# Kernel optimization log

Hardware: AMD Instinct MI355X
Metric: run time of the kernel (lower is better)

## Reference

```python
import jax, jax.numpy as jnp
import numpy as np

VOCAB = 32000
ROUTE_BIAS = 10.0  # weight on the deterministic one-hot route vs mu logits


def setup_inputs() -> dict:
    key = jax.random.key(0)
    k1, k2, k3, k4, k5, k6 = jax.random.split(key, 6)
    B, S, H = 2, 4096, 1024
    E, Ie = 8, 512  # intermediate_size=4096 -> expert_intermediate=512, fused dim=2*Ie=1024
    return {
        "hidden_states": jax.random.normal(k1, (B, S, H), dtype=jnp.float32),
        "token_ids": jax.random.randint(k2, (B, S), 0, VOCAB),
        "mu": jax.random.normal(k3, (B, S, H), dtype=jnp.float32),
        "gate_up_proj": jax.random.normal(k4, (E, H, 2 * Ie), dtype=jnp.float32) * 0.02,
        "down_proj": jax.random.normal(k5, (E, Ie, H), dtype=jnp.float32) * 0.02,
        "mu_router_w": jax.random.normal(k6, (E, H), dtype=jnp.float32) * 0.02,
    }


def reference(hidden_states, token_ids, mu, gate_up_proj, down_proj, mu_router_w):
    B, S, H = hidden_states.shape
    E, _, F2 = gate_up_proj.shape
    Ie = F2 // 2
    N = B * S

    # deterministic token->expert routing, optionally perturbed by mu logits
    token_to_expert = jnp.arange(VOCAB, dtype=jnp.int32) % E
    base_expert = token_to_expert[jnp.clip(token_ids, 0, VOCAB - 1)]      # [B,S]
    mu_logits = jnp.einsum('bsh,eh->bse', mu, mu_router_w)                 # [B,S,E]
    combined = jax.nn.one_hot(base_expert, E, dtype=mu_logits.dtype) * ROUTE_BIAS + mu_logits
    expert_ids = jnp.argmax(combined, axis=-1).reshape(N)                  # [N]

    x = hidden_states.reshape(N, H)
    tok = jnp.arange(N)

    # compute per-expert GEMM then select per-token expert output
    # (same math as gathering the full weight slab per token, without the
    #  N*H*2Ie gathered-weight blowup of the original torch code)
    gu_all = jnp.einsum('nh,ehf->enf', x, gate_up_proj)                    # [E,N,2Ie]
    gu = gu_all[expert_ids, tok]                                           # [N,2Ie]
    gate, up = gu[:, :Ie], gu[:, Ie:]
    inter = jax.nn.silu(gate) * up                                         # [N,Ie]

    z_all = jnp.einsum('ni,eih->enh', inter, down_proj)                    # [E,N,H]
    out = z_all[expert_ids, tok].reshape(B, S, H)
    return out
```

## Files before the change

kernel.cpp:

```cpp
#include <hip/hip_runtime.h>
#include <hip/hip_bf16.h>
#include <stdint.h>

typedef __bf16 bf16x8 __attribute__((ext_vector_type(8)));
typedef float f32x4 __attribute__((ext_vector_type(4)));

#define ROUTE_BIAS_F 10.0f
#define VOCAB_SZ 32000

__device__ __forceinline__ unsigned short f2bf(float f) {
    union { float f; unsigned u; } v; v.f = f;
    unsigned u = v.u;
    unsigned r = u + 0x7FFFu + ((u >> 16) & 1u);
    return (unsigned short)(r >> 16);
}
__device__ __forceinline__ float bf2f(unsigned short s) {
    union { unsigned u; float f; } v; v.u = ((unsigned)s) << 16;
    return v.f;
}
__device__ __forceinline__ void ld16(const unsigned short* g, unsigned short* l) {
    __builtin_amdgcn_global_load_lds(
        (const __attribute__((address_space(1))) void*)g,
        (__attribute__((address_space(3))) void*)l, 16, 0, 0);
}

__global__ void k_convert_bf16(const float* __restrict__ in,
                               unsigned short* __restrict__ out, int n) {
    int i = (blockIdx.x * blockDim.x + threadIdx.x) * 4;
    if (i + 3 < n) {
        float4 f = *(const float4*)(in + i);
        ushort4 o;
        o.x = f2bf(f.x); o.y = f2bf(f.y); o.z = f2bf(f.z); o.w = f2bf(f.w);
        *(ushort4*)(out + i) = o;
    } else {
        for (; i < n; ++i) out[i] = f2bf(in[i]);
    }
}

__global__ void k_transpose_bf16(const float* __restrict__ in,
                                 unsigned short* __restrict__ out, int R, int C) {
    __shared__ float tile[32][33];
    int e = blockIdx.z;
    const float* inp = in + (size_t)e * R * C;
    unsigned short* outp = out + (size_t)e * R * C;
    int c0 = blockIdx.x * 32, r0 = blockIdx.y * 32;
    int tx = threadIdx.x, ty = threadIdx.y;
#pragma unroll
    for (int k = 0; k < 32; k += 8)
        tile[ty + k][tx] = inp[(size_t)(r0 + ty + k) * C + c0 + tx];
    __syncthreads();
#pragma unroll
    for (int k = 0; k < 32; k += 8)
        outp[(size_t)(c0 + ty + k) * R + r0 + tx] = f2bf(tile[tx][ty + k]);
}

__global__ void k_logits(const float* __restrict__ mu, const int* __restrict__ tok_ids,
                         const float* __restrict__ rw, int H, int N,
                         int* __restrict__ eids) {
    int lane = threadIdx.x & 63;
    int wv   = threadIdx.x >> 6;
    int tok  = blockIdx.x * 4 + wv;
    if (tok >= N) return;
    float acc[8];
#pragma unroll
    for (int e = 0; e < 8; ++e) acc[e] = 0.f;
    const float* m = mu + (size_t)tok * H;
    for (int h = lane; h < H; h += 64) {
        float mv = m[h];
#pragma unroll
        for (int e = 0; e < 8; ++e) acc[e] += mv * rw[e * H + h];
    }
#pragma unroll
    for (int e = 0; e < 8; ++e) {
        float v = acc[e];
#pragma unroll
        for (int off = 32; off > 0; off >>= 1) v += __shfl_xor(v, off);
        acc[e] = v;
    }
    if (lane == 0) {
        int t = tok_ids[tok];
        if (t < 0) t = 0;
        if (t > VOCAB_SZ - 1) t = VOCAB_SZ - 1;
        int be = t % 8;
        float best = -1e30f; int bi = 0;
#pragma unroll
        for (int e = 0; e < 8; ++e) {
            float v = acc[e] + (e == be ? ROUTE_BIAS_F : 0.f);
            if (v > best) { best = v; bi = e; }
        }
        eids[tok] = bi;
    }
}

__global__ void k_count(const int* __restrict__ eids,
                        int* __restrict__ blockcnt, int N) {
    __shared__ int cnt[8];
    int tid = threadIdx.x;
    if (tid < 8) cnt[tid] = 0;
    __syncthreads();
    int tok = blockIdx.x * 256 + tid;
    int lane = tid & 63;
    int eid = (tok < N) ? eids[tok] : -1;
#pragma unroll
    for (int e = 0; e < 8; ++e) {
        unsigned long long m = __ballot(eid == e);
        if (lane == 0 && m) atomicAdd(&cnt[e], __popcll(m));
    }
    __syncthreads();
    if (tid < 8) blockcnt[blockIdx.x * 8 + tid] = cnt[tid];
}

__global__ void k_scan(const int* __restrict__ blockcnt,
                       int* __restrict__ counts, int* __restrict__ base_,
                       int* __restrict__ offs, int NB) {
    __shared__ int tot[8];
    int lane = threadIdx.x;
    int e = lane >> 3, g = lane & 7;
    int v[4];
    int s = 0;
#pragma unroll
    for (int i = 0; i < 4; ++i) { v[i] = s; s += blockcnt[(g * 4 + i) * 8 + e]; }
    int inc = s;
#pragma unroll
    for (int d = 1; d < 8; d <<= 1) {
        int t = __shfl_up(inc, d);
        if (g >= d) inc += t;
    }
    int excl = inc - s;
#pragma unroll
    for (int i = 0; i < 4; ++i) offs[(g * 4 + i) * 8 + e] = excl + v[i];
    if (g == 7) { counts[e] = inc; tot[e] = inc; }
    __syncthreads();
    if (lane == 0) {
        int s2 = 0;
#pragma unroll
        for (int i = 0; i < 8; ++i) { base_[i] = s2; s2 += tot[i]; }
    }
}

__global__ void k_scatter(const int* __restrict__ eids,
                          const int* __restrict__ offs,
                          int* __restrict__ list, int N) {
    __shared__ int wavecnt[4][8];
    int tid = threadIdx.x;
    int lane = tid & 63, wv = tid >> 6;
    int tok = blockIdx.x * 256 + tid;
    int eid = (tok < N) ? eids[tok] : -1;
    unsigned long long below = (1ull << lane) - 1ull;
    int myrank = 0;
#pragma unroll
    for (int e = 0; e < 8; ++e) {
        unsigned long long m = __ballot(eid == e);
        if (lane == 0) wavecnt[wv][e] = __popcll(m);
        if (eid == e) myrank = __popcll(m & below);
    }
    __syncthreads();
    if (eid >= 0) {
        int pre = 0;
        for (int w = 0; w < wv; ++w) pre += wavecnt[w][eid];
        int pos = offs[blockIdx.x * 8 + eid] + pre + myrank;
        list[eid * N + pos] = tok;
    }
}

#define TM 64
#define TN 128
#define TK 64

__global__ __launch_bounds__(256, 4) void k_gemm_gateup(
    const unsigned short* __restrict__ X,
    const unsigned short* __restrict__ Wt,
    unsigned short* __restrict__ IT,
    const int* __restrict__ counts, const int* __restrict__ base_,
    const int* __restrict__ list, int N, int H, int Ie) {
    int bid = blockIdx.x;
    int e = bid & 7;
    int t = bid >> 3;
    int nt = t & 7;
    int mt = t >> 3;
    int cnt = counts[e];
    int m0 = mt * TM;
    if (m0 >= cnt) return;
    int F2 = 2 * Ie;

    __shared__ __align__(16) unsigned short As[TM * TK];
    __shared__ __align__(16) unsigned short Bs[TN * TK];

    int tid = threadIdx.x;
    int lane = tid & 63, wv = tid >> 6;
    int wm = (wv >> 1) * 32, wn = (wv & 1) * 64;

    int rowg = lane >> 3;
    int sl   = (lane & 7) ^ rowg;

    const unsigned short* ag[2];
    const unsigned short* bg[4];
#pragma unroll
    for (int i = 0; i < 2; ++i) {
        int r = wv * 16 + i * 8 + rowg;
        int gr = m0 + r;
        int tokrow = (gr < cnt) ? list[e * N + gr] : 0;
        ag[i] = X + (size_t)tokrow * H + sl * 8;
    }
#pragma unroll
    for (int i = 0; i < 4; ++i) {
        int r = wv * 32 + i * 8 + rowg;
        int wrow = (r & 1) * Ie + nt * 64 + (r >> 1);
        bg[i] = Wt + ((size_t)e * F2 + wrow) * H + sl * 8;
    }

    f32x4 acc[2][4];
#pragma unroll
    for (int i = 0; i < 2; ++i)
#pragma unroll
        for (int j = 0; j < 4; ++j) acc[i][j] = (f32x4)(0.f);

    int q = lane >> 4, m = lane & 15;
    int sw = m & 7;

    for (int k0 = 0; k0 < H; k0 += TK) {
#pragma unroll
        for (int i = 0; i < 2; ++i)
            ld16(ag[i] + k0, &As[(wv * 16 + i * 8) * TK]);
#pragma unroll
        for (int i = 0; i < 4; ++i)
            ld16(bg[i] + k0, &Bs[(wv * 32 + i * 8) * TK]);
        __syncthreads();
#pragma unroll
        for (int ks = 0; ks < TK; ks += 32) {
            int kc = ks >> 3;
            int ck = ((kc + q) ^ sw) << 3;
            bf16x8 af[2], bfr[4];
#pragma unroll
            for (int im = 0; im < 2; ++im)
                af[im] = *(const bf16x8*)&As[(wm + m + im * 16) * TK + ck];
#pragma unroll
            for (int in_ = 0; in_ < 4; ++in_)
                bfr[in_] = *(const bf16x8*)&Bs[(wn + m + in_ * 16) * TK + ck];
#pragma unroll
            for (int im = 0; im < 2; ++im)
#pragma unroll
                for (int in_ = 0; in_ < 4; ++in_)
                    acc[im][in_] = __builtin_amdgcn_mfma_f32_16x16x32_bf16(
                        af[im], bfr[in_], acc[im][in_], 0, 0, 0);
        }
        __syncthreads();
    }

    int b = base_[e];
    int nt64 = nt * 64;
#pragma unroll
    for (int im = 0; im < 2; ++im) {
#pragma unroll
        for (int j = 0; j < 4; ++j) {
            int row = wm + im * 16 + q * 4 + j;
            int gr = m0 + row;
#pragma unroll
            for (int in_ = 0; in_ < 4; ++in_) {
                float v = acc[im][in_][j];
                float u = __shfl_xor(v, 1);
                float g = v;
                float s = g / (1.f + __expf(-g));
                float res = s * u;
                if (!(lane & 1) && gr < cnt) {
                    int oc = nt64 + ((wn + in_ * 16 + m) >> 1);
                    IT[(size_t)(b + gr) * Ie + oc] = f2bf(res);
                }
            }
        }
    }
}

__global__ __launch_bounds__(256, 4) void k_gemm_down(
    const unsigned short* __restrict__ IT,
    const unsigned short* __restrict__ Wt,
    float* __restrict__ OUT,
    const int* __restrict__ counts, const int* __restrict__ base_,
    const int* __restrict__ list, int N, int Ie, int H) {
    int bid = blockIdx.x;
    int e = bid & 7;
    int t = bid >> 3;
    int nt = t & 7;
    int mt = t >> 3;
    int cnt = counts[e];
    int m0 = mt * TM;
    if (m0 >= cnt) return;
    int n0 = nt * TN;
    int b = base_[e];

    __shared__ __align__(16) unsigned short As[TM * TK];
    __shared__ __align__(16) unsigned short Bs[TN * TK];

    int tid = threadIdx.x;
    int lane = tid & 63, wv = tid >> 6;
    int wm = (wv >> 1) * 32, wn = (wv & 1) * 64;

    int rowg = lane >> 3;
    int sl   = (lane & 7) ^ rowg;

    const unsigned short* We = Wt + ((size_t)e * H + n0) * Ie;
    const unsigned short* ag[2];
    const unsigned short* bg[4];
#pragma unroll
    for (int i = 0; i < 2; ++i) {
        int r = wv * 16 + i * 8 + rowg;
        int gr = m0 + r;
        int arow = (gr < cnt) ? (b + gr) : b;
        ag[i] = IT + (size_t)arow * Ie + sl * 8;
    }
#pragma unroll
    for (int i = 0; i < 4; ++i) {
        int r = wv * 32 + i * 8 + rowg;
        bg[i] = We + (size_t)r * Ie + sl * 8;
    }

    f32x4 acc[2][4];
#pragma unroll
    for (int i = 0; i < 2; ++i)
#pragma unroll
        for (int j = 0; j < 4; ++j) acc[i][j] = (f32x4)(0.f);

    int q = lane >> 4, m = lane & 15;
    int sw = m & 7;

    for (int k0 = 0; k0 < Ie; k0 += TK) {
#pragma unroll
        for (int i = 0; i < 2; ++i)
            ld16(ag[i] + k0, &As[(wv * 16 + i * 8) * TK]);
#pragma unroll
        for (int i = 0; i < 4; ++i)
            ld16(bg[i] + k0, &Bs[(wv * 32 + i * 8) * TK]);
        __syncthreads();
#pragma unroll
        for (int ks = 0; ks < TK; ks += 32) {
            int kc = ks >> 3;
            int ck = ((kc + q) ^ sw) << 3;
            bf16x8 af[2], bfr[4];
#pragma unroll
            for (int im = 0; im < 2; ++im)
                af[im] = *(const bf16x8*)&As[(wm + m + im * 16) * TK + ck];
#pragma unroll
            for (int in_ = 0; in_ < 4; ++in_)
                bfr[in_] = *(const bf16x8*)&Bs[(wn + m + in_ * 16) * TK + ck];
#pragma unroll
            for (int im = 0; im < 2; ++im)
#pragma unroll
                for (int in_ = 0; in_ < 4; ++in_)
                    acc[im][in_] = __builtin_amdgcn_mfma_f32_16x16x32_bf16(
                        af[im], bfr[in_], acc[im][in_], 0, 0, 0);
        }
        __syncthreads();
    }

#pragma unroll
    for (int im = 0; im < 2; ++im) {
#pragma unroll
        for (int j = 0; j < 4; ++j) {
            int row = wm + im * 16 + q * 4 + j;
            int gr = m0 + row;
            if (gr < cnt) {
                int tok = list[e * N + gr];
                float* orow = OUT + (size_t)tok * H + n0;
#pragma unroll
                for (int in_ = 0; in_ < 4; ++in_) {
                    int col = wn + in_ * 16 + m;
                    orow[col] = acc[im][in_][j];
                }
            }
        }
    }
}

extern "C" void kernel_launch(void* const* d_in, const int* in_sizes, int n_in,
                              void* d_out, int out_size, void* d_ws, size_t ws_size,
                              hipStream_t stream) {
    const float* hidden   = (const float*)d_in[0];
    const int*   tok_ids  = (const int*)d_in[1];
    const float* mu       = (const float*)d_in[2];
    const float* gup      = (const float*)d_in[3];
    const float* dnp      = (const float*)d_in[4];
    const float* rw       = (const float*)d_in[5];
    float* out = (float*)d_out;

    int N  = in_sizes[1];
    int H  = in_sizes[0] / N;
    int E  = in_sizes[5] / H;
    int F2 = in_sizes[3] / (E * H);
    int Ie = F2 / 2;

    int NB = (N + 255) / 256;

    char* ws = (char*)d_ws;
    size_t o = 0;
    auto alloc = [&](size_t sz) {
        size_t r = o;
        o += (sz + 255) & ~(size_t)255;
        return r;
    };
    int* counts   = (int*)(ws + alloc((size_t)E * 4));
    int* base_    = (int*)(ws + alloc((size_t)E * 4));
    int* eids     = (int*)(ws + alloc((size_t)N * 4));
    int* blockcnt = (int*)(ws + alloc((size_t)NB * 8 * 4));
    int* offs     = (int*)(ws + alloc((size_t)NB * 8 * 4));
    int* list     = (int*)(ws + alloc((size_t)E * N * 4));
    unsigned short* xb   = (unsigned short*)(ws + alloc((size_t)N * H * 2));
    unsigned short* wgut = (unsigned short*)(ws + alloc((size_t)E * F2 * H * 2));
    unsigned short* wdnt = (unsigned short*)(ws + alloc((size_t)E * H * Ie * 2));
    unsigned short* it   = (unsigned short*)(ws + alloc((size_t)N * Ie * 2));

    k_convert_bf16<<<dim3((N * H / 4 + 255) / 256), dim3(256), 0, stream>>>(hidden, xb, N * H);

    dim3 tb(32, 8);
    k_transpose_bf16<<<dim3(F2 / 32, H / 32, E), tb, 0, stream>>>(gup, wgut, H, F2);
    k_transpose_bf16<<<dim3(H / 32, Ie / 32, E), tb, 0, stream>>>(dnp, wdnt, Ie, H);

    k_logits<<<dim3((N + 3) / 4), dim3(256), 0, stream>>>(mu, tok_ids, rw, H, N, eids);
    k_count<<<dim3(NB), dim3(256), 0, stream>>>(eids, blockcnt, N);
    k_scan<<<dim3(1), dim3(64), 0, stream>>>(blockcnt, counts, base_, offs, NB);
    k_scatter<<<dim3(NB), dim3(256), 0, stream>>>(eids, offs, list, N);

    int MT = (N + TM - 1) / TM;
    k_gemm_gateup<<<dim3(E * MT * (Ie / 64)), dim3(256), 0, stream>>>(
        xb, wgut, it, counts, base_, list, N, H, Ie);

    k_gemm_down<<<dim3(E * MT * (H / TN)), dim3(256), 0, stream>>>(
        it, wdnt, out, counts, base_, list, N, Ie, H);
}
```

Before: 227.5 us.

## Fuse bf16 convert into router logits, merge transposes, use 2-wave GEMM blocks

Hidden-state bf16 conversion is folded into the router-logit kernel, which now reads mu and the router weights with float4 loads, removing one launch and a separate pass over the activations. The two weight transposes are merged into a single launch covering both weight tensors. Both expert GEMMs move from 4 waves of 32x64 tiles to 2 waves each computing 64x64, doubling per-wave MFMA work and register use and halving threads per block, with launch bounds lowered accordingly. The higher register count may reduce occupancy.

```diff
diff --git a/kernel.cpp b/kernel.cpp
--- a/kernel.cpp
+++ b/kernel.cpp
@@ -24,51 +24,35 @@
         (__attribute__((address_space(3))) void*)l, 16, 0, 0);
 }
 
-__global__ void k_convert_bf16(const float* __restrict__ in,
-                               unsigned short* __restrict__ out, int n) {
-    int i = (blockIdx.x * blockDim.x + threadIdx.x) * 4;
-    if (i + 3 < n) {
-        float4 f = *(const float4*)(in + i);
-        ushort4 o;
-        o.x = f2bf(f.x); o.y = f2bf(f.y); o.z = f2bf(f.z); o.w = f2bf(f.w);
-        *(ushort4*)(out + i) = o;
-    } else {
-        for (; i < n; ++i) out[i] = f2bf(in[i]);
-    }
-}
-
-__global__ void k_transpose_bf16(const float* __restrict__ in,
-                                 unsigned short* __restrict__ out, int R, int C) {
-    __shared__ float tile[32][33];
-    int e = blockIdx.z;
-    const float* inp = in + (size_t)e * R * C;
-    unsigned short* outp = out + (size_t)e * R * C;
-    int c0 = blockIdx.x * 32, r0 = blockIdx.y * 32;
-    int tx = threadIdx.x, ty = threadIdx.y;
-#pragma unroll
-    for (int k = 0; k < 32; k += 8)
-        tile[ty + k][tx] = inp[(size_t)(r0 + ty + k) * C + c0 + tx];
-    __syncthreads();
-#pragma unroll
-    for (int k = 0; k < 32; k += 8)
-        outp[(size_t)(c0 + ty + k) * R + r0 + tx] = f2bf(tile[tx][ty + k]);
-}
-
-__global__ void k_logits(const float* __restrict__ mu, const int* __restrict__ tok_ids,
-                         const float* __restrict__ rw, int H, int N,
-                         int* __restrict__ eids) {
+__global__ void k_prep(const float* __restrict__ hidden, const float* __restrict__ mu,
+                       const int* __restrict__ tok_ids, const float* __restrict__ rw,
+                       unsigned short* __restrict__ xb, int* __restrict__ eids,
+                       int H, int N) {
     int lane = threadIdx.x & 63;
     int wv   = threadIdx.x >> 6;
     int tok  = blockIdx.x * 4 + wv;
     if (tok >= N) return;
+    const float4* hp = (const float4*)(hidden + (size_t)tok * H);
+    const float4* mp = (const float4*)(mu + (size_t)tok * H);
+    const float4* rp = (const float4*)rw;
+    ushort4* xp = (ushort4*)(xb + (size_t)tok * H);
+    int H4 = H >> 2;
     float acc[8];
 #pragma unroll
     for (int e = 0; e < 8; ++e) acc[e] = 0.f;
-    const float* m = mu + (size_t)tok * H;
-    for (int h = lane; h < H; h += 64) {
-        float mv = m[h];
-#pragma unroll
-        for (int e = 0; e < 8; ++e) acc[e] += mv * rw[e * H + h];
+#pragma unroll
+    for (int j = 0; j < 4; ++j) {
+        int idx = lane + 64 * j;
+        float4 h4 = hp[idx];
+        ushort4 o;
+        o.x = f2bf(h4.x); o.y = f2bf(h4.y); o.z = f2bf(h4.z); o.w = f2bf(h4.w);
+        xp[idx] = o;
+        float4 m4 = mp[idx];
+#pragma unroll
+        for (int e = 0; e < 8; ++e) {
+            float4 w4 = rp[e * H4 + idx];
+            acc[e] += m4.x * w4.x + m4.y * w4.y + m4.z * w4.z + m4.w * w4.w;
+        }
     }
 #pragma unroll
     for (int e = 0; e < 8; ++e) {
@@ -90,6 +74,26 @@
         }
         eids[tok] = bi;
     }
+}
+
+__global__ void k_transpose_all(const float* __restrict__ gup, const float* __restrict__ dnp,
+                                unsigned short* __restrict__ wgut, unsigned short* __restrict__ wdnt,
+                                int H, int F2, int Ie) {
+    __shared__ float tile[32][33];
+    int z = blockIdx.z;
+    const float* inp; unsigned short* outp; int R, C;
+    if (z < 8) { R = H; C = F2; inp = gup + (size_t)z * R * C;       outp = wgut + (size_t)z * R * C; }
+    else       { R = Ie; C = H; inp = dnp + (size_t)(z - 8) * R * C; outp = wdnt + (size_t)(z - 8) * R * C; }
+    int c0 = blockIdx.x * 32, r0 = blockIdx.y * 32;
+    if (r0 >= R || c0 >= C) return;
+    int tx = threadIdx.x, ty = threadIdx.y;
+#pragma unroll
+    for (int k = 0; k < 32; k += 8)
+        tile[ty + k][tx] = inp[(size_t)(r0 + ty + k) * C + c0 + tx];
+    __syncthreads();
+#pragma unroll
+    for (int k = 0; k < 32; k += 8)
+        outp[(size_t)(c0 + ty + k) * R + r0 + tx] = f2bf(tile[tx][ty + k]);
 }
 
 __global__ void k_count(const int* __restrict__ eids,
@@ -167,7 +171,7 @@
 #define TN 128
 #define TK 64
 
-__global__ __launch_bounds__(256, 4) void k_gemm_gateup(
+__global__ __launch_bounds__(128, 3) void k_gemm_gateup(
     const unsigned short* __restrict__ X,
     const unsigned short* __restrict__ Wt,
     unsigned short* __restrict__ IT,
@@ -188,30 +192,30 @@
 
     int tid = threadIdx.x;
     int lane = tid & 63, wv = tid >> 6;
-    int wm = (wv >> 1) * 32, wn = (wv & 1) * 64;
+    int wn = wv * 64;
 
     int rowg = lane >> 3;
     int sl   = (lane & 7) ^ rowg;
 
-    const unsigned short* ag[2];
-    const unsigned short* bg[4];
-#pragma unroll
-    for (int i = 0; i < 2; ++i) {
-        int r = wv * 16 + i * 8 + rowg;
+    const unsigned short* ag[4];
+    const unsigned short* bg[8];
+#pragma unroll
+    for (int i = 0; i < 4; ++i) {
+        int r = wv * 32 + i * 8 + rowg;
         int gr = m0 + r;
         int tokrow = (gr < cnt) ? list[e * N + gr] : 0;
         ag[i] = X + (size_t)tokrow * H + sl * 8;
     }
 #pragma unroll
-    for (int i = 0; i < 4; ++i) {
-        int r = wv * 32 + i * 8 + rowg;
+    for (int i = 0; i < 8; ++i) {
+        int r = wv * 64 + i * 8 + rowg;
         int wrow = (r & 1) * Ie + nt * 64 + (r >> 1);
         bg[i] = Wt + ((size_t)e * F2 + wrow) * H + sl * 8;
     }
 
-    f32x4 acc[2][4];
-#pragma unroll
-    for (int i = 0; i < 2; ++i)
+    f32x4 acc[4][4];
+#pragma unroll
+    for (int i = 0; i < 4; ++i)
 #pragma unroll
         for (int j = 0; j < 4; ++j) acc[i][j] = (f32x4)(0.f);
 
@@ -220,25 +224,25 @@
 
     for (int k0 = 0; k0 < H; k0 += TK) {
 #pragma unroll
-        for (int i = 0; i < 2; ++i)
-            ld16(ag[i] + k0, &As[(wv * 16 + i * 8) * TK]);
-#pragma unroll
         for (int i = 0; i < 4; ++i)
-            ld16(bg[i] + k0, &Bs[(wv * 32 + i * 8) * TK]);
+            ld16(ag[i] + k0, &As[(wv * 32 + i * 8) * TK]);
+#pragma unroll
+        for (int i = 0; i < 8; ++i)
+            ld16(bg[i] + k0, &Bs[(wv * 64 + i * 8) * TK]);
         __syncthreads();
 #pragma unroll
         for (int ks = 0; ks < TK; ks += 32) {
             int kc = ks >> 3;
             int ck = ((kc + q) ^ sw) << 3;
-            bf16x8 af[2], bfr[4];
-#pragma unroll
-            for (int im = 0; im < 2; ++im)
-                af[im] = *(const bf16x8*)&As[(wm + m + im * 16) * TK + ck];
+            bf16x8 af[4], bfr[4];
+#pragma unroll
+            for (int im = 0; im < 4; ++im)
+                af[im] = *(const bf16x8*)&As[(m + im * 16) * TK + ck];
 #pragma unroll
             for (int in_ = 0; in_ < 4; ++in_)
                 bfr[in_] = *(const bf16x8*)&Bs[(wn + m + in_ * 16) * TK + ck];
 #pragma unroll
-            for (int im = 0; im < 2; ++im)
+            for (int im = 0; im < 4; ++im)
 #pragma unroll
                 for (int in_ = 0; in_ < 4; ++in_)
                     acc[im][in_] = __builtin_amdgcn_mfma_f32_16x16x32_bf16(
@@ -250,10 +254,10 @@
     int b = base_[e];
     int nt64 = nt * 64;
 #pragma unroll
-    for (int im = 0; im < 2; ++im) {
+    for (int im = 0; im < 4; ++im) {
 #pragma unroll
         for (int j = 0; j < 4; ++j) {
-            int row = wm + im * 16 + q * 4 + j;
+            int row = im * 16 + q * 4 + j;
             int gr = m0 + row;
 #pragma unroll
             for (int in_ = 0; in_ < 4; ++in_) {
@@ -271,7 +275,7 @@
     }
 }
 
-__global__ __launch_bounds__(256, 4) void k_gemm_down(
+__global__ __launch_bounds__(128, 3) void k_gemm_down(
     const unsigned short* __restrict__ IT,
     const unsigned short* __restrict__ Wt,
     float* __restrict__ OUT,
@@ -293,30 +297,30 @@
 
     int tid = threadIdx.x;
     int lane = tid & 63, wv = tid >> 6;
-    int wm = (wv >> 1) * 32, wn = (wv & 1) * 64;
+    int wn = wv * 64;
 
     int rowg = lane >> 3;
     int sl   = (lane & 7) ^ rowg;
 
     const unsigned short* We = Wt + ((size_t)e * H + n0) * Ie;
-    const unsigned short* ag[2];
-    const unsigned short* bg[4];
-#pragma unroll
-    for (int i = 0; i < 2; ++i) {
-        int r = wv * 16 + i * 8 + rowg;
+    const unsigned short* ag[4];
+    const unsigned short* bg[8];
+#pragma unroll
+    for (int i = 0; i < 4; ++i) {
+        int r = wv * 32 + i * 8 + rowg;
         int gr = m0 + r;
         int arow = (gr < cnt) ? (b + gr) : b;
         ag[i] = IT + (size_t)arow * Ie + sl * 8;
     }
 #pragma unroll
-    for (int i = 0; i < 4; ++i) {
-        int r = wv * 32 + i * 8 + rowg;
+    for (int i = 0; i < 8; ++i) {
+        int r = wv * 64 + i * 8 + rowg;
         bg[i] = We + (size_t)r * Ie + sl * 8;
     }
 
-    f32x4 acc[2][4];
-#pragma unroll
-    for (int i = 0; i < 2; ++i)
+    f32x4 acc[4][4];
+#pragma unroll
+    for (int i = 0; i < 4; ++i)
 #pragma unroll
         for (int j = 0; j < 4; ++j) acc[i][j] = (f32x4)(0.f);
 
@@ -325,25 +329,25 @@
 
     for (int k0 = 0; k0 < Ie; k0 += TK) {
 #pragma unroll
-        for (int i = 0; i < 2; ++i)
-            ld16(ag[i] + k0, &As[(wv * 16 + i * 8) * TK]);
-#pragma unroll
         for (int i = 0; i < 4; ++i)
-            ld16(bg[i] + k0, &Bs[(wv * 32 + i * 8) * TK]);
+            ld16(ag[i] + k0, &As[(wv * 32 + i * 8) * TK]);
+#pragma unroll
+        for (int i = 0; i < 8; ++i)
+            ld16(bg[i] + k0, &Bs[(wv * 64 + i * 8) * TK]);
         __syncthreads();
 #pragma unroll
         for (int ks = 0; ks < TK; ks += 32) {
             int kc = ks >> 3;
             int ck = ((kc + q) ^ sw) << 3;
-            bf16x8 af[2], bfr[4];
-#pragma unroll
-            for (int im = 0; im < 2; ++im)
-                af[im] = *(const bf16x8*)&As[(wm + m + im * 16) * TK + ck];
+            bf16x8 af[4], bfr[4];
+#pragma unroll
+            for (int im = 0; im < 4; ++im)
+                af[im] = *(const bf16x8*)&As[(m + im * 16) * TK + ck];
 #pragma unroll
             for (int in_ = 0; in_ < 4; ++in_)
                 bfr[in_] = *(const bf16x8*)&Bs[(wn + m + in_ * 16) * TK + ck];
 #pragma unroll
-            for (int im = 0; im < 2; ++im)
+            for (int im = 0; im < 4; ++im)
 #pragma unroll
                 for (int in_ = 0; in_ < 4; ++in_)
                     acc[im][in_] = __builtin_amdgcn_mfma_f32_16x16x32_bf16(
@@ -353,10 +357,10 @@
     }
 
 #pragma unroll
-    for (int im = 0; im < 2; ++im) {
+    for (int im = 0; im < 4; ++im) {
 #pragma unroll
         for (int j = 0; j < 4; ++j) {
-            int row = wm + im * 16 + q * 4 + j;
+            int row = im * 16 + q * 4 + j;
             int gr = m0 + row;
             if (gr < cnt) {
                 int tok = list[e * N + gr];
@@ -408,21 +412,18 @@
     unsigned short* wdnt = (unsigned short*)(ws + alloc((size_t)E * H * Ie * 2));
     unsigned short* it   = (unsigned short*)(ws + alloc((size_t)N * Ie * 2));
 
-    k_convert_bf16<<<dim3((N * H / 4 + 255) / 256), dim3(256), 0, stream>>>(hidden, xb, N * H);
-
-    dim3 tb(32, 8);
-    k_transpose_bf16<<<dim3(F2 / 32, H / 32, E), tb, 0, stream>>>(gup, wgut, H, F2);
-    k_transpose_bf16<<<dim3(H / 32, Ie / 32, E), tb, 0, stream>>>(dnp, wdnt, Ie, H);
-
-    k_logits<<<dim3((N + 3) / 4), dim3(256), 0, stream>>>(mu, tok_ids, rw, H, N, eids);
+    k_prep<<<dim3((N + 3) / 4), dim3(256), 0, stream>>>(hidden, mu, tok_ids, rw, xb, eids, H, N);
+
+    k_transpose_all<<<dim3(32, 32, 16), dim3(32, 8), 0, stream>>>(gup, dnp, wgut, wdnt, H, F2, Ie);
+
     k_count<<<dim3(NB), dim3(256), 0, stream>>>(eids, blockcnt, N);
     k_scan<<<dim3(1), dim3(64), 0, stream>>>(blockcnt, counts, base_, offs, NB);
     k_scatter<<<dim3(NB), dim3(256), 0, stream>>>(eids, offs, list, N);
 
     int MT = (N + TM - 1) / TM;
-    k_gemm_gateup<<<dim3(E * MT * (Ie / 64)), dim3(256), 0, stream>>>(
+    k_gemm_gateup<<<dim3(E * MT * (Ie / 64)), dim3(128), 0, stream>>>(
         xb, wgut, it, counts, base_, list, N, H, Ie);
 
-    k_gemm_down<<<dim3(E * MT * (H / TN)), dim3(256), 0, stream>>>(
+    k_gemm_down<<<dim3(E * MT * (H / TN)), dim3(128), 0, stream>>>(
         it, wdnt, out, counts, base_, list, N, Ie, H);
 }
```

After: 224.9 us. About the same (-1.1%).
